# Kernel tuning notes

Measured on AMD Instinct MI355X. Metric: run time of the kernel, lower is better.

The kernel has to match this reference:

```python
import jax, jax.numpy as jnp
import numpy as np

EPS = 1e-12  # torch F.normalize eps


def _l2norm(x):
    n = jnp.linalg.norm(x, axis=-1, keepdims=True)
    return x / jnp.maximum(n, EPS)


def setup_inputs() -> dict:
    key = jax.random.key(0)
    k1, k2 = jax.random.split(key)
    B, Lq, Lk, D = 128, 32, 128, 128
    left_emb = jax.random.normal(k1, (B, Lq, D), dtype=jnp.float32)
    right_emb = jax.random.normal(k2, (B, Lk, D), dtype=jnp.float32)
    pos_idx = jnp.arange(B, dtype=jnp.int64)
    logit_scale = jnp.asarray(np.log(1.0 / 0.07), dtype=jnp.float32)  # scalar param
    return {"left_emb": left_emb, "right_emb": right_emb,
            "logit_scale": logit_scale, "pos_idx": pos_idx}


def reference(left_emb, right_emb, logit_scale, pos_idx):
    # maxsim_colbert: normalize token embeddings, cross-sim, max over doc
    # tokens, sum over query tokens -> [B, B] logits, then CE loss.
    l = _l2norm(left_emb)   # [B, Lq, D]
    r = _l2norm(right_emb)  # [B, Lk, D]
    sims = jnp.einsum('xik,yjk->xyij', l, r)        # [B, B, Lq, Lk]
    sim = sims.max(axis=-1).sum(axis=-1)            # [B, B]
    logits = jnp.exp(logit_scale) * sim
    logp = jax.nn.log_softmax(logits, axis=1)
    B = logits.shape[0]
    loss = -jnp.mean(logp[jnp.arange(B), pos_idx])
    return loss
```

## Files before the change

kernel.cpp:

```cpp
#include <hip/hip_runtime.h>
#include <hip/hip_bf16.h>

typedef short bf16x8 __attribute__((ext_vector_type(8)));
typedef float f32x16 __attribute__((ext_vector_type(16)));
typedef unsigned short u16;

#define B 128
#define LQ 32
#define LK 128
#define D 128


static __device__ inline u16 f2bf_rne(float f) {
  union { float f; unsigned u; } v; v.f = f;
  unsigned r = v.u + 0x7fffu + ((v.u >> 16) & 1u);
  return (u16)(r >> 16);
}

__global__ __launch_bounds__(256) void normalize_kernel(
    const float* __restrict__ left, const float* __restrict__ right,
    char* __restrict__ lbf, char* __restrict__ rbf) {
  int wave = (blockIdx.x * blockDim.x + threadIdx.x) >> 6;
  int lane = threadIdx.x & 63;
  const int n_l = B * LQ;
  const float* src; char* dst;
  if (wave < n_l) {
    src = left + (size_t)wave * D;
    dst = lbf + (wave >> 5) * 8192 + (wave & 31) * 16;
  } else {
    int row = wave - n_l;
    src = right + (size_t)row * D;
    dst = rbf + (row >> 7) * 32768 + ((row >> 5) & 3) * 8192 + (row & 31) * 16;
  }
  float2 v = *reinterpret_cast<const float2*>(src + lane * 2);
  float ss = v.x * v.x + v.y * v.y;
#pragma unroll
  for (int off = 1; off < 64; off <<= 1) ss += __shfl_xor(ss, off);
  float inv = 1.0f / fmaxf(sqrtf(ss), 1e-12f);
  unsigned packed = (unsigned)f2bf_rne(v.x * inv) |
                    ((unsigned)f2bf_rne(v.y * inv) << 16);
  *reinterpret_cast<unsigned*>(
      dst + (lane >> 3) * 1024 + ((lane >> 2) & 1) * 512 + (lane & 3) * 4) = packed;
}

__global__ __launch_bounds__(256, 2) void maxsim_kernel(
    const char* __restrict__ lbf, const char* __restrict__ rbf,
    float* __restrict__ sims) {
  const int lane = threadIdx.x & 63;
  const int wv   = threadIdx.x >> 6;
  const int xg   = blockIdx.x >> 5;
  const int yg   = blockIdx.x & 31;
  const int x0   = xg * 8 + wv * 2;
  const int lane16 = lane * 16;

  bf16x8 bfr[2][8];
#pragma unroll
  for (int xi = 0; xi < 2; ++xi)
#pragma unroll
    for (int ks = 0; ks < 8; ++ks)
      bfr[xi][ks] = *reinterpret_cast<const bf16x8*>(
          lbf + (x0 + xi) * 8192 + ks * 1024 + lane16);

  f32x16 z;
#pragma unroll
  for (int t = 0; t < 16; ++t) z[t] = 0.f;

  const char* rb0 = rbf + (size_t)(yg * 4) * 32768;

#define LOADA(dst, s_next)                                                   \
  {                                                                          \
    const char* nb = rb0 + (s_next) * 8192;                                  \
    _Pragma("unroll")                                                        \
    for (int ks = 0; ks < 8; ++ks)                                           \
      dst[ks] = *reinterpret_cast<const bf16x8*>(nb + ks * 1024 + lane16);   \
  }

#define MFMAB(srcA)                                                          \
  __builtin_amdgcn_s_setprio(1);                                             \
  a0 = __builtin_amdgcn_mfma_f32_32x32x16_bf16(srcA[0], bfr[0][0], z, 0, 0, 0); \
  a1 = __builtin_amdgcn_mfma_f32_32x32x16_bf16(srcA[0], bfr[1][0], z, 0, 0, 0); \
  _Pragma("unroll")                                                          \
  for (int ks = 1; ks < 8; ++ks) {                                           \
    a0 = __builtin_amdgcn_mfma_f32_32x32x16_bf16(srcA[ks], bfr[0][ks], a0, 0, 0, 0); \
    a1 = __builtin_amdgcn_mfma_f32_32x32x16_bf16(srcA[ks], bfr[1][ks], a1, 0, 0, 0); \
  }                                                                          \
  __builtin_amdgcn_s_setprio(0);

#define FOLD()                                                               \
  _Pragma("unroll")                                                          \
  for (int t = 0; t < 16; t += 4) {                                          \
    cm0 = fmaxf(cm0, fmaxf(fmaxf(a0[t], a0[t + 1]), fmaxf(a0[t + 2], a0[t + 3]))); \
    cm1 = fmaxf(cm1, fmaxf(fmaxf(a1[t], a1[t + 1]), fmaxf(a1[t + 2], a1[t + 3]))); \
  }

#define STEP(s, CUR, PF)                                                     \
  if ((s) + 2 < 16) LOADA(PF, (s) + 2);                                      \
  MFMAB(CUR);                                                                \
  FOLD();

#define EPI(yy)                                                              \
  cm0 = fmaxf(cm0, __shfl_xor(cm0, 32));                                     \
  cm1 = fmaxf(cm1, __shfl_xor(cm1, 32));                                     \
  _Pragma("unroll")                                                          \
  for (int off = 1; off <= 16; off <<= 1) {                                  \
    cm0 += __shfl_xor(cm0, off);                                             \
    cm1 += __shfl_xor(cm1, off);                                             \
  }                                                                          \
  if (lane == 0) {                                                           \
    sims[(x0 + 0) * B + (yg * 4 + (yy))] = cm0;                              \
    sims[(x0 + 1) * B + (yg * 4 + (yy))] = cm1;                              \
  }

  bf16x8 p0[8], p1[8], p2[8];
  f32x16 a0, a1;
  float cm0, cm1;

  LOADA(p0, 0);
  LOADA(p1, 1);

  cm0 = cm1 = -3.0e38f;
  STEP(0,  p0, p2); STEP(1,  p1, p0); STEP(2,  p2, p1); STEP(3,  p0, p2);
  EPI(0);
  cm0 = cm1 = -3.0e38f;
  STEP(4,  p1, p0); STEP(5,  p2, p1); STEP(6,  p0, p2); STEP(7,  p1, p0);
  EPI(1);
  cm0 = cm1 = -3.0e38f;
  STEP(8,  p2, p1); STEP(9,  p0, p2); STEP(10, p1, p0); STEP(11, p2, p1);
  EPI(2);
  cm0 = cm1 = -3.0e38f;
  STEP(12, p0, p2); STEP(13, p1, p0); STEP(14, p2, p1); STEP(15, p0, p1);
  EPI(3);

#undef LOADA
#undef MFMAB
#undef FOLD
#undef STEP
#undef EPI
}

__global__ __launch_bounds__(1024) void loss_kernel(
    const float* __restrict__ sims, const float* __restrict__ logit_scale,
    const int* __restrict__ pos_idx, float* __restrict__ out) {
  __shared__ float red[16];
  const int lane = threadIdx.x & 63;
  const int wv   = threadIdx.x >> 6;
  const float scale = expf(logit_scale[0]);
  float local = 0.f;
#pragma unroll
  for (int rr = 0; rr < 8; ++rr) {
    const int x = wv * 8 + rr;
    const float* row = sims + x * B;
    float a = row[lane], b2 = row[64 + lane];
    float m = fmaxf(a, b2);
#pragma unroll
    for (int off = 1; off < 64; off <<= 1) m = fmaxf(m, __shfl_xor(m, off));
    float ml = scale * m;
    float e = expf(scale * a - ml) + expf(scale * b2 - ml);
#pragma unroll
    for (int off = 1; off < 64; off <<= 1) e += __shfl_xor(e, off);
    int pos = pos_idx[x];
    float pv = __shfl(pos < 64 ? a : b2, pos & 63);
    local += -(scale * pv - ml - logf(e));
  }
  if (lane == 0) red[wv] = local;
  __syncthreads();
  if (threadIdx.x == 0) {
    float t = 0.f;
#pragma unroll
    for (int i = 0; i < 16; ++i) t += red[i];
    out[0] = t / (float)B;
  }
}

extern "C" void kernel_launch(void* const* d_in, const int* in_sizes, int n_in,
                              void* d_out, int out_size, void* d_ws, size_t ws_size,
                              hipStream_t stream) {
  const float* left  = (const float*)d_in[0];
  const float* right = (const float*)d_in[1];
  const float* ls    = (const float*)d_in[2];
  const int*   pos   = (const int*)d_in[3];
  float* out = (float*)d_out;

  char* ws  = (char*)d_ws;
  char* lbf = ws;
  char* rbf = ws + (size_t)(1 << 20);
  float* sims = (float*)(ws + (size_t)(5 << 20));

  int waves = B * LQ + B * LK;
  normalize_kernel<<<waves / 4, 256, 0, stream>>>(left, right, lbf, rbf);
  maxsim_kernel<<<512, 256, 0, stream>>>(lbf, rbf, sims);
  loss_kernel<<<1, 1024, 0, stream>>>(sims, ls, pos, out);
}
```

Before: 34.96 us.

## Halve per-block y-tile in maxsim and batch five rows per wave in normalize

The maxsim kernel now has each block handle 2 right-side documents instead of 4, doubling the grid to 1024 blocks. This gives more parallelism across CUs but reloads the left fragments twice as often. The normalize kernel is restructured so each wave processes four right rows and one left row with all loads issued up front, using a fixed 1024-block grid. This batching is meant to improve memory-level parallelism.

```diff
diff --git a/kernel.cpp b/kernel.cpp
--- a/kernel.cpp
+++ b/kernel.cpp
@@ -20,27 +20,46 @@
 __global__ __launch_bounds__(256) void normalize_kernel(
     const float* __restrict__ left, const float* __restrict__ right,
     char* __restrict__ lbf, char* __restrict__ rbf) {
-  int wave = (blockIdx.x * blockDim.x + threadIdx.x) >> 6;
-  int lane = threadIdx.x & 63;
-  const int n_l = B * LQ;
-  const float* src; char* dst;
-  if (wave < n_l) {
-    src = left + (size_t)wave * D;
-    dst = lbf + (wave >> 5) * 8192 + (wave & 31) * 16;
-  } else {
-    int row = wave - n_l;
-    src = right + (size_t)row * D;
-    dst = rbf + (row >> 7) * 32768 + ((row >> 5) & 3) * 8192 + (row & 31) * 16;
-  }
-  float2 v = *reinterpret_cast<const float2*>(src + lane * 2);
-  float ss = v.x * v.x + v.y * v.y;
-#pragma unroll
-  for (int off = 1; off < 64; off <<= 1) ss += __shfl_xor(ss, off);
-  float inv = 1.0f / fmaxf(sqrtf(ss), 1e-12f);
-  unsigned packed = (unsigned)f2bf_rne(v.x * inv) |
-                    ((unsigned)f2bf_rne(v.y * inv) << 16);
-  *reinterpret_cast<unsigned*>(
-      dst + (lane >> 3) * 1024 + ((lane >> 2) & 1) * 512 + (lane & 3) * 4) = packed;
+  const int lane = threadIdx.x & 63;
+  const int wv   = threadIdx.x >> 6;
+  const int b    = blockIdx.x;
+  const int yg   = b & 63, xg = b >> 6;
+
+  int   rrow[5];
+  const float* srcs[5];
+#pragma unroll
+  for (int t = 0; t < 4; ++t) {
+    rrow[t] = yg * 256 + xg * 16 + wv * 4 + t;
+    srcs[t] = right + (size_t)rrow[t] * D;
+  }
+  rrow[4] = b * 4 + wv;
+  srcs[4] = left + (size_t)rrow[4] * D;
+
+  float2 v[5];
+#pragma unroll
+  for (int t = 0; t < 5; ++t)
+    v[t] = *reinterpret_cast<const float2*>(srcs[t] + lane * 2);
+
+  const unsigned lslot =
+      (lane >> 3) * 1024u + ((lane >> 2) & 1) * 512u + (lane & 3) * 4u;
+#pragma unroll
+  for (int t = 0; t < 5; ++t) {
+    float ss = v[t].x * v[t].x + v[t].y * v[t].y;
+#pragma unroll
+    for (int off = 1; off < 64; off <<= 1) ss += __shfl_xor(ss, off);
+    float inv = 1.0f / fmaxf(sqrtf(ss), 1e-12f);
+    unsigned packed = (unsigned)f2bf_rne(v[t].x * inv) |
+                      ((unsigned)f2bf_rne(v[t].y * inv) << 16);
+    char* dst;
+    if (t < 4) {
+      int r2 = rrow[t];
+      dst = rbf + (r2 >> 7) * 32768 + ((r2 >> 5) & 3) * 8192 + (r2 & 31) * 16;
+    } else {
+      int lr = rrow[4];
+      dst = lbf + (lr >> 5) * 8192 + (lr & 31) * 16;
+    }
+    *reinterpret_cast<unsigned*>(dst + lslot) = packed;
+  }
 }
 
 __global__ __launch_bounds__(256, 2) void maxsim_kernel(
@@ -48,8 +67,8 @@
     float* __restrict__ sims) {
   const int lane = threadIdx.x & 63;
   const int wv   = threadIdx.x >> 6;
-  const int xg   = blockIdx.x >> 5;
-  const int yg   = blockIdx.x & 31;
+  const int xg   = blockIdx.x >> 6;
+  const int yg   = blockIdx.x & 63;
   const int x0   = xg * 8 + wv * 2;
   const int lane16 = lane * 16;
 
@@ -65,7 +84,7 @@
 #pragma unroll
   for (int t = 0; t < 16; ++t) z[t] = 0.f;
 
-  const char* rb0 = rbf + (size_t)(yg * 4) * 32768;
+  const char* rb0 = rbf + (size_t)yg * 2 * 32768;
 
 #define LOADA(dst, s_next)                                                   \
   {                                                                          \
@@ -94,7 +113,7 @@
   }
 
 #define STEP(s, CUR, PF)                                                     \
-  if ((s) + 2 < 16) LOADA(PF, (s) + 2);                                      \
+  if ((s) + 2 < 8) LOADA(PF, (s) + 2);                                       \
   MFMAB(CUR);                                                                \
   FOLD();
 
@@ -107,8 +126,8 @@
     cm1 += __shfl_xor(cm1, off);                                             \
   }                                                                          \
   if (lane == 0) {                                                           \
-    sims[(x0 + 0) * B + (yg * 4 + (yy))] = cm0;                              \
-    sims[(x0 + 1) * B + (yg * 4 + (yy))] = cm1;                              \
+    sims[(x0 + 0) * B + (yg * 2 + (yy))] = cm0;                              \
+    sims[(x0 + 1) * B + (yg * 2 + (yy))] = cm1;                              \
   }
 
   bf16x8 p0[8], p1[8], p2[8];
@@ -119,17 +138,11 @@
   LOADA(p1, 1);
 
   cm0 = cm1 = -3.0e38f;
-  STEP(0,  p0, p2); STEP(1,  p1, p0); STEP(2,  p2, p1); STEP(3,  p0, p2);
+  STEP(0, p0, p2); STEP(1, p1, p0); STEP(2, p2, p1); STEP(3, p0, p2);
   EPI(0);
   cm0 = cm1 = -3.0e38f;
-  STEP(4,  p1, p0); STEP(5,  p2, p1); STEP(6,  p0, p2); STEP(7,  p1, p0);
+  STEP(4, p1, p0); STEP(5, p2, p1); STEP(6, p0, p2); STEP(7, p1, p0);
   EPI(1);
-  cm0 = cm1 = -3.0e38f;
-  STEP(8,  p2, p1); STEP(9,  p0, p2); STEP(10, p1, p0); STEP(11, p2, p1);
-  EPI(2);
-  cm0 = cm1 = -3.0e38f;
-  STEP(12, p0, p2); STEP(13, p1, p0); STEP(14, p2, p1); STEP(15, p0, p1);
-  EPI(3);
 
 #undef LOADA
 #undef MFMAB
@@ -186,8 +199,7 @@
   char* rbf = ws + (size_t)(1 << 20);
   float* sims = (float*)(ws + (size_t)(5 << 20));
 
-  int waves = B * LQ + B * LK;
-  normalize_kernel<<<waves / 4, 256, 0, stream>>>(left, right, lbf, rbf);
-  maxsim_kernel<<<512, 256, 0, stream>>>(lbf, rbf, sims);
+  normalize_kernel<<<1024, 256, 0, stream>>>(left, right, lbf, rbf);
+  maxsim_kernel<<<1024, 256, 0, stream>>>(lbf, rbf, sims);
   loss_kernel<<<1, 1024, 0, stream>>>(sims, ls, pos, out);
 }
```

Result: no change. 35.46 us (+1.4%).
